# Kernel tuning notes

Hardware: AMD Instinct MI355X
Metric: run time of the kernel (lower is better)

The kernel has to match this reference:

```python
import jax, jax.numpy as jnp
import numpy as np

N_NODES = 100000
N_EDGES = 1600000
D_FEAT = 64
UNITS = [128, 128]


def setup_inputs() -> dict:
    key = jax.random.key(0)
    ks = jax.random.split(key, 8)
    row = jax.random.randint(ks[0], (N_EDGES,), 0, N_NODES, dtype=jnp.int32)
    col = jax.random.randint(ks[1], (N_EDGES,), 0, N_NODES, dtype=jnp.int32)
    vals = jax.random.uniform(ks[2], (N_EDGES,), dtype=jnp.float32)
    H = jax.random.normal(ks[3], (N_NODES, D_FEAT), dtype=jnp.float32)
    W1 = jax.random.normal(ks[4], (D_FEAT, UNITS[0]), dtype=jnp.float32) * (1.0 / np.sqrt(D_FEAT))
    b1 = jnp.zeros((UNITS[0],), dtype=jnp.float32)
    W2 = jax.random.normal(ks[5], (UNITS[0], UNITS[1]), dtype=jnp.float32) * (1.0 / np.sqrt(UNITS[0]))
    b2 = jnp.zeros((UNITS[1],), dtype=jnp.float32)
    return {"row": row, "col": col, "vals": vals, "H": H,
            "W1": W1, "b1": b1, "W2": W2, "b2": b2}


def _spmm(row, col, vals, H, n_nodes):
    # sparse A (COO) @ dense H: gather source rows, scale, scatter-add to dest
    return jax.ops.segment_sum(vals[:, None] * H[col], row, num_segments=n_nodes)


def reference(row, col, vals, H, W1, b1, W2, b2):
    n = H.shape[0]
    # layer 0: AH @ W1 + b1, relu (source bug: relu applied since i < num_units-1)
    AH = _spmm(row, col, vals, H, n)
    H1 = jax.nn.relu(AH @ W1 + b1)
    # layer 1: same structure, also relu per source's activation condition
    AH1 = _spmm(row, col, vals, H1, n)
    H2 = jax.nn.relu(AH1 @ W2 + b2)
    return H2
```

## Files before the change

kernel.cpp:

```cpp
#include <hip/hip_runtime.h>


#define NFEAT 64
#define NHID 128
#define BSHIFT 9
#define BROWS (1 << BSHIFT)
#define NB_MAX 256

typedef __attribute__((ext_vector_type(8))) short bf16x8;
typedef __attribute__((ext_vector_type(4))) float f32x4;
typedef __attribute__((ext_vector_type(2))) float f32x2;

__device__ __forceinline__ unsigned short f2bf(float x) {
  unsigned u = __float_as_uint(x);
  unsigned r = (u + 0x7FFFu + ((u >> 16) & 1u)) >> 16;
  return (unsigned short)r;
}
__device__ __forceinline__ unsigned pack2(float a, float b) {
  return (unsigned)f2bf(a) | ((unsigned)f2bf(b) << 16);
}

__device__ __forceinline__ unsigned pk_fp8x4(float a, float b, float c, float d) {
  int w = __builtin_amdgcn_cvt_pk_fp8_f32(a, b, 0, false);
  w = __builtin_amdgcn_cvt_pk_fp8_f32(c, d, w, true);
  return (unsigned)w;
}
__device__ __forceinline__ unsigned char f2fp8(float x) {
  return (unsigned char)(__builtin_amdgcn_cvt_pk_fp8_f32(x, 0.f, 0, false) & 0xFF);
}

__device__ __forceinline__ void acc16(f32x2* a, uint4 q, float v) {
  f32x2 vv = {v, v};
  a[0] += vv * __builtin_amdgcn_cvt_pk_f32_fp8(q.x, false);
  a[1] += vv * __builtin_amdgcn_cvt_pk_f32_fp8(q.x, true);
  a[2] += vv * __builtin_amdgcn_cvt_pk_f32_fp8(q.y, false);
  a[3] += vv * __builtin_amdgcn_cvt_pk_f32_fp8(q.y, true);
  a[4] += vv * __builtin_amdgcn_cvt_pk_f32_fp8(q.z, false);
  a[5] += vv * __builtin_amdgcn_cvt_pk_f32_fp8(q.z, true);
  a[6] += vv * __builtin_amdgcn_cvt_pk_f32_fp8(q.w, false);
  a[7] += vv * __builtin_amdgcn_cvt_pk_f32_fp8(q.w, true);
}

__global__ __launch_bounds__(256) void prep_kernel(
    const float* __restrict__ H, const float* __restrict__ W1,
    const float* __restrict__ W2, unsigned char* __restrict__ Hf8,
    unsigned short* __restrict__ Wsw1, unsigned short* __restrict__ Wsw2,
    int n8) {
  const int total = n8 + 64 * 128 + 128 * 128;
  for (int w = blockIdx.x * 256 + threadIdx.x; w < total; w += gridDim.x * 256) {
    if (w < n8) {
      float4 a = ((const float4*)H)[2 * w];
      float4 b = ((const float4*)H)[2 * w + 1];
      ((uint2*)Hf8)[w] = make_uint2(pk_fp8x4(a.x, a.y, a.z, a.w),
                                    pk_fp8x4(b.x, b.y, b.z, b.w));
    } else {
      int idx = w - n8;
      const float* W = W1;
      unsigned short* Wsw = Wsw1;
      if (idx >= 64 * 128) {
        idx -= 64 * 128;
        W = W2;
        Wsw = Wsw2;
      }
      int j = idx & 7, q = (idx >> 3) & 3, nn = (idx >> 5) & 127, kt = idx >> 12;
      int k = kt * 32 + q * 8 + j;
      Wsw[idx] = f2bf(W[(size_t)k * 128 + nn]);
    }
  }
}

__global__ __launch_bounds__(256) void bhist_kernel(
    const int* __restrict__ row, int* __restrict__ bcnt, int n_edges, int nb) {
  __shared__ int h[NB_MAX];
  for (int i = threadIdx.x; i < NB_MAX; i += 256) h[i] = 0;
  __syncthreads();
  for (int e = blockIdx.x * 256 + threadIdx.x; e < n_edges; e += gridDim.x * 256)
    atomicAdd(&h[row[e] >> BSHIFT], 1);
  __syncthreads();
  for (int i = threadIdx.x; i < nb; i += 256)
    if (h[i]) atomicAdd(&bcnt[i], h[i]);
}

__global__ __launch_bounds__(NB_MAX) void bscan_kernel(
    const int* __restrict__ bcnt, int* __restrict__ bbase, int* __restrict__ cur,
    int* __restrict__ row_ptr, int nb, int n) {
  __shared__ int sm[NB_MAX];
  int t = threadIdx.x;
  int v = (t < nb) ? bcnt[t] : 0;
  sm[t] = v;
  __syncthreads();
  for (int off = 1; off < NB_MAX; off <<= 1) {
    int u = (t >= off) ? sm[t - off] : 0;
    __syncthreads();
    sm[t] += u;
    __syncthreads();
  }
  if (t < nb) {
    bbase[t] = sm[t] - v;
    cur[t] = sm[t] - v;
  }
  if (t == nb - 1) {
    bbase[nb] = sm[t];
    row_ptr[n] = sm[t];
  }
}

__global__ __launch_bounds__(256) void partition_kernel(
    const int* __restrict__ row, const int* __restrict__ col,
    const float* __restrict__ vals, int* __restrict__ cur,
    int2* __restrict__ bedge, int n_edges) {
  __shared__ int h[NB_MAX], base[NB_MAX], rk[NB_MAX];
  for (int i = threadIdx.x; i < NB_MAX; i += 256) {
    h[i] = 0;
    rk[i] = 0;
  }
  __syncthreads();
  const int start = blockIdx.x * 256 + threadIdx.x;
  const int step = gridDim.x * 256;
  for (int e = start; e < n_edges; e += step)
    atomicAdd(&h[row[e] >> BSHIFT], 1);
  __syncthreads();
  for (int i = threadIdx.x; i < NB_MAX; i += 256)
    base[i] = h[i] ? atomicAdd(&cur[i], h[i]) : 0;
  __syncthreads();
  for (int e = start; e < n_edges; e += step) {
    int r = row[e];
    int b = r >> BSHIFT;
    int rl = r & (BROWS - 1);
    int p = base[b] + atomicAdd(&rk[b], 1);
    bedge[p] = make_int2((rl << 17) | col[e], __float_as_int(vals[e]));
  }
}

__global__ __launch_bounds__(512) void bucket_csr_kernel(
    const int* __restrict__ bbase, const int2* __restrict__ bedge,
    int* __restrict__ row_ptr, int2* __restrict__ sedge, int n) {
  __shared__ int cnt[BROWS];
  __shared__ int sm[BROWS];
  const int b = blockIdx.x;
  const int t = threadIdx.x;
  const int beg = bbase[b], end = bbase[b + 1];
  cnt[t] = 0;
  __syncthreads();
  for (int j = beg + t; j < end; j += 512)
    atomicAdd(&cnt[((unsigned)bedge[j].x) >> 17], 1);
  __syncthreads();
  int v = cnt[t];
  sm[t] = v;
  __syncthreads();
  for (int off = 1; off < BROWS; off <<= 1) {
    int u = (t >= off) ? sm[t - off] : 0;
    __syncthreads();
    sm[t] += u;
    __syncthreads();
  }
  {
    int incl = sm[t];
    __syncthreads();
    sm[t] = incl - v;
  }
  int r = (b << BSHIFT) + t;
  if (r < n) row_ptr[r] = beg + sm[t];
  cnt[t] = 0;
  __syncthreads();
  for (int j = beg + t; j < end; j += 512) {
    int2 ev = bedge[j];
    int rl = ((unsigned)ev.x) >> 17;
    int rank = atomicAdd(&cnt[rl], 1);
    sedge[beg + sm[rl] + rank] = make_int2(ev.x & 0x1FFFF, ev.y);
  }
}

__global__ __launch_bounds__(256) void spmm64_csr_f8(
    const int* __restrict__ row_ptr, const int2* __restrict__ sedge,
    const unsigned char* __restrict__ Hf8, unsigned short* __restrict__ outbf,
    int n) {
  int tid = blockIdx.x * 256 + threadIdx.x;
  int r = tid >> 2;
  int f = tid & 3;
  if (r >= n) return;
  const uint4* Hq = (const uint4*)Hf8;
  int beg = row_ptr[r], end = row_ptr[r + 1];
  f32x2 a[8];
#pragma unroll
  for (int i = 0; i < 8; ++i) a[i] = (f32x2){0.f, 0.f};
  int j = beg;
  if ((j & 1) && j < end) {
    int2 ev = sedge[j];
    uint4 q = Hq[ev.x * 4 + f];
    acc16(a, q, __int_as_float(ev.y));
    ++j;
  }
  for (; j + 4 <= end; j += 4) {
    int4 p0 = ((const int4*)sedge)[j >> 1];
    int4 p1 = ((const int4*)sedge)[(j >> 1) + 1];
    uint4 q0 = Hq[p0.x * 4 + f];
    uint4 q1 = Hq[p0.z * 4 + f];
    uint4 q2 = Hq[p1.x * 4 + f];
    uint4 q3 = Hq[p1.z * 4 + f];
    acc16(a, q0, __int_as_float(p0.y));
    acc16(a, q1, __int_as_float(p0.w));
    acc16(a, q2, __int_as_float(p1.y));
    acc16(a, q3, __int_as_float(p1.w));
  }
  for (; j < end; ++j) {
    int2 ev = sedge[j];
    uint4 q = Hq[ev.x * 4 + f];
    acc16(a, q, __int_as_float(ev.y));
  }
  uint4 o0 = make_uint4(pack2(a[0].x, a[0].y), pack2(a[1].x, a[1].y),
                        pack2(a[2].x, a[2].y), pack2(a[3].x, a[3].y));
  uint4 o1 = make_uint4(pack2(a[4].x, a[4].y), pack2(a[5].x, a[5].y),
                        pack2(a[6].x, a[6].y), pack2(a[7].x, a[7].y));
  ((uint4*)outbf)[(size_t)r * 8 + f * 2] = o0;
  ((uint4*)outbf)[(size_t)r * 8 + f * 2 + 1] = o1;
}

__global__ __launch_bounds__(256) void spmm128_csr_f8(
    const int* __restrict__ row_ptr, const int2* __restrict__ sedge,
    const unsigned char* __restrict__ Hf8, unsigned short* __restrict__ outbf,
    int n) {
  int tid = blockIdx.x * 256 + threadIdx.x;
  int r = tid >> 3;
  int f = tid & 7;
  if (r >= n) return;
  const uint4* Hq = (const uint4*)Hf8;
  int beg = row_ptr[r], end = row_ptr[r + 1];
  f32x2 a[8];
#pragma unroll
  for (int i = 0; i < 8; ++i) a[i] = (f32x2){0.f, 0.f};
  int j = beg;
  if ((j & 1) && j < end) {
    int2 ev = sedge[j];
    uint4 q = Hq[ev.x * 8 + f];
    acc16(a, q, __int_as_float(ev.y));
    ++j;
  }
  for (; j + 4 <= end; j += 4) {
    int4 p0 = ((const int4*)sedge)[j >> 1];
    int4 p1 = ((const int4*)sedge)[(j >> 1) + 1];
    uint4 q0 = Hq[p0.x * 8 + f];
    uint4 q1 = Hq[p0.z * 8 + f];
    uint4 q2 = Hq[p1.x * 8 + f];
    uint4 q3 = Hq[p1.z * 8 + f];
    acc16(a, q0, __int_as_float(p0.y));
    acc16(a, q1, __int_as_float(p0.w));
    acc16(a, q2, __int_as_float(p1.y));
    acc16(a, q3, __int_as_float(p1.w));
  }
  for (; j < end; ++j) {
    int2 ev = sedge[j];
    uint4 q = Hq[ev.x * 8 + f];
    acc16(a, q, __int_as_float(ev.y));
  }
  uint4 o0 = make_uint4(pack2(a[0].x, a[0].y), pack2(a[1].x, a[1].y),
                        pack2(a[2].x, a[2].y), pack2(a[3].x, a[3].y));
  uint4 o1 = make_uint4(pack2(a[4].x, a[4].y), pack2(a[5].x, a[5].y),
                        pack2(a[6].x, a[6].y), pack2(a[7].x, a[7].y));
  ((uint4*)outbf)[(size_t)r * 16 + f * 2] = o0;
  ((uint4*)outbf)[(size_t)r * 16 + f * 2 + 1] = o1;
}

template <int K, int OUTMODE>
__global__ __launch_bounds__(256) void gemm_mfma_relu(
    const unsigned short* __restrict__ Abf,
    const unsigned short* __restrict__ Wsw,
    const float* __restrict__ b, void* __restrict__ out_v, int n) {
  constexpr int KT = K / 32;
  const int lane = threadIdx.x & 63;
  const int wave = threadIdx.x >> 6;
  const int m = lane & 15;
  const int quad = lane >> 4;
  const int r0 = blockIdx.x * 64 + wave * 16;

  bf16x8 bfr[KT][8];
#pragma unroll
  for (int kt = 0; kt < KT; ++kt)
#pragma unroll
    for (int c = 0; c < 8; ++c)
      bfr[kt][c] = *(const bf16x8*)(Wsw + ((size_t)(kt * 128 + c * 16 + m)) * 32 + quad * 8);

  f32x4 acc[8];
#pragma unroll
  for (int c = 0; c < 8; ++c) acc[c] = (f32x4){0.f, 0.f, 0.f, 0.f};

  int row = r0 + m;
  if (row >= n) row = n - 1;
  const uint4* Arow = (const uint4*)(Abf + (size_t)row * K);
#pragma unroll
  for (int kt = 0; kt < KT; ++kt) {
    bf16x8 a = *(const bf16x8*)&Arow[kt * 4 + quad];
#pragma unroll
    for (int c = 0; c < 8; ++c)
      acc[c] = __builtin_amdgcn_mfma_f32_16x16x32_bf16(a, bfr[kt][c], acc[c], 0, 0, 0);
  }

#pragma unroll
  for (int c = 0; c < 8; ++c) {
    float bias = b[c * 16 + m];
#pragma unroll
    for (int i = 0; i < 4; ++i) {
      int rr = r0 + quad * 4 + i;
      if (rr >= n) continue;
      float v = fmaxf(acc[c][i] + bias, 0.f);
      if (OUTMODE == 2)
        ((unsigned char*)out_v)[(size_t)rr * 128 + c * 16 + m] = f2fp8(v);
      else
        ((float*)out_v)[(size_t)rr * 128 + c * 16 + m] = v;
    }
  }
}

__global__ __launch_bounds__(256) void spmm64_atomic(
    const int* __restrict__ row, const int* __restrict__ col,
    const float* __restrict__ vals, const float* __restrict__ Hin,
    float* __restrict__ out, int n_edges) {
  int tid = blockIdx.x * 256 + threadIdx.x;
  int e = tid >> 4, f = tid & 15;
  if (e >= n_edges) return;
  int c = col[e], r = row[e];
  float v = vals[e];
  float4 h = ((const float4*)Hin)[(size_t)c * 16 + f];
  float* o = out + (size_t)r * 64 + f * 4;
  atomicAdd(o + 0, v * h.x);
  atomicAdd(o + 1, v * h.y);
  atomicAdd(o + 2, v * h.z);
  atomicAdd(o + 3, v * h.w);
}

__global__ __launch_bounds__(256) void spmm128_atomic(
    const int* __restrict__ row, const int* __restrict__ col,
    const float* __restrict__ vals, const float* __restrict__ Hin,
    float* __restrict__ out, int n_edges) {
  int tid = blockIdx.x * 256 + threadIdx.x;
  int e = tid >> 5, f = tid & 31;
  if (e >= n_edges) return;
  int c = col[e], r = row[e];
  float v = vals[e];
  float4 h = ((const float4*)Hin)[(size_t)c * 32 + f];
  float* o = out + (size_t)r * 128 + f * 4;
  atomicAdd(o + 0, v * h.x);
  atomicAdd(o + 1, v * h.y);
  atomicAdd(o + 2, v * h.z);
  atomicAdd(o + 3, v * h.w);
}

template <int K>
__global__ __launch_bounds__(256) void gemm_tiled_relu(
    const float* __restrict__ A, const float* __restrict__ W,
    const float* __restrict__ b, float* __restrict__ out, int n) {
  constexpr int KB = 32;
  constexpr int RP = 132;
  __shared__ float As[KB][RP];
  __shared__ float Ws[KB][128];
  const int t = threadIdx.x;
  const int tx = t & 15, ty = t >> 4;
  const int r0 = blockIdx.x * 128;
  float4 acc0[8], acc1[8];
#pragma unroll
  for (int i = 0; i < 8; ++i) {
    acc0[i] = make_float4(0.f, 0.f, 0.f, 0.f);
    acc1[i] = make_float4(0.f, 0.f, 0.f, 0.f);
  }
  for (int k0 = 0; k0 < K; k0 += KB) {
#pragma unroll
    for (int q = 0; q < 4; ++q) {
      int f = q * 256 + t;
      int kk = f >> 5, cv = f & 31;
      ((float4*)&Ws[kk][0])[cv] = ((const float4*)(W + (size_t)(k0 + kk) * 128))[cv];
    }
#pragma unroll
    for (int q = 0; q < 4; ++q) {
      int f = q * 256 + t;
      int r = f >> 3, kv = f & 7;
      float4 av = make_float4(0.f, 0.f, 0.f, 0.f);
      if (r0 + r < n) av = ((const float4*)(A + (size_t)(r0 + r) * K + k0))[kv];
      As[4 * kv + 0][r] = av.x;
      As[4 * kv + 1][r] = av.y;
      As[4 * kv + 2][r] = av.z;
      As[4 * kv + 3][r] = av.w;
    }
    __syncthreads();
#pragma unroll
    for (int k = 0; k < KB; ++k) {
      float4 w0 = *((const float4*)&Ws[k][4 * tx]);
      float4 w1 = *((const float4*)&Ws[k][64 + 4 * tx]);
#pragma unroll
      for (int i = 0; i < 8; ++i) {
        float a = As[k][ty + 16 * i];
        acc0[i].x = fmaf(a, w0.x, acc0[i].x);
        acc0[i].y = fmaf(a, w0.y, acc0[i].y);
        acc0[i].z = fmaf(a, w0.z, acc0[i].z);
        acc0[i].w = fmaf(a, w0.w, acc0[i].w);
        acc1[i].x = fmaf(a, w1.x, acc1[i].x);
        acc1[i].y = fmaf(a, w1.y, acc1[i].y);
        acc1[i].z = fmaf(a, w1.z, acc1[i].z);
        acc1[i].w = fmaf(a, w1.w, acc1[i].w);
      }
    }
    __syncthreads();
  }
  float4 bb0 = ((const float4*)b)[tx];
  float4 bb1 = ((const float4*)(b + 64))[tx];
#pragma unroll
  for (int i = 0; i < 8; ++i) {
    int r = r0 + ty + 16 * i;
    if (r >= n) continue;
    float4 o0, o1;
    o0.x = fmaxf(acc0[i].x + bb0.x, 0.f);
    o0.y = fmaxf(acc0[i].y + bb0.y, 0.f);
    o0.z = fmaxf(acc0[i].z + bb0.z, 0.f);
    o0.w = fmaxf(acc0[i].w + bb0.w, 0.f);
    o1.x = fmaxf(acc1[i].x + bb1.x, 0.f);
    o1.y = fmaxf(acc1[i].y + bb1.y, 0.f);
    o1.z = fmaxf(acc1[i].z + bb1.z, 0.f);
    o1.w = fmaxf(acc1[i].w + bb1.w, 0.f);
    ((float4*)(out + (size_t)r * 128))[tx] = o0;
    ((float4*)(out + (size_t)r * 128 + 64))[tx] = o1;
  }
}

extern "C" void kernel_launch(void* const* d_in, const int* in_sizes, int n_in,
                              void* d_out, int out_size, void* d_ws, size_t ws_size,
                              hipStream_t stream) {
  const int* row = (const int*)d_in[0];
  const int* col = (const int*)d_in[1];
  const float* vals = (const float*)d_in[2];
  const float* H = (const float*)d_in[3];
  const float* W1 = (const float*)d_in[4];
  const float* b1 = (const float*)d_in[5];
  const float* W2 = (const float*)d_in[6];
  const float* b2 = (const float*)d_in[7];
  float* out = (float*)d_out;

  const int n_edges = in_sizes[0];
  const int n_nodes = in_sizes[3] / NFEAT;
  const int nb = (n_nodes + BROWS - 1) / BROWS;
  const int mfma_grid = (n_nodes + 63) / 64;

  size_t off = 0;
  char* base = (char*)d_ws;
  char* slab0 = base;
  size_t slab0_sz = (size_t)n_edges * 8;
  size_t ah1_sz = (size_t)n_nodes * NHID * 2;
  if (ah1_sz > slab0_sz) slab0_sz = ah1_sz;
  off += slab0_sz;
  unsigned char* Hf8 = (unsigned char*)(base + off);   off += (size_t)n_nodes * NFEAT;
  unsigned char* H1f8 = (unsigned char*)(base + off);  off += (size_t)n_nodes * NHID;
  unsigned short* AHbf = (unsigned short*)(base + off); off += (size_t)n_nodes * NFEAT * 2;
  int2* sedge = (int2*)(base + off);  off += (size_t)n_edges * 8;
  unsigned short* Wsw1 = (unsigned short*)(base + off); off += 64 * 128 * 2;
  unsigned short* Wsw2 = (unsigned short*)(base + off); off += 128 * 128 * 2;
  int* bcnt = (int*)(base + off);     off += NB_MAX * 4;
  int* bbase = (int*)(base + off);    off += (NB_MAX + 1) * 4;
  int* cur = (int*)(base + off);      off += NB_MAX * 4;
  int* row_ptr = (int*)(base + off);  off += ((size_t)n_nodes + 1) * 4;
  const size_t needed = off;
  int2* bedge = (int2*)slab0;
  unsigned short* AH1bf = (unsigned short*)slab0;

  if (ws_size >= needed && nb <= NB_MAX && n_nodes <= (1 << 17)) {
    hipMemsetAsync(bcnt, 0, NB_MAX * sizeof(int), stream);
    bhist_kernel<<<256, 256, 0, stream>>>(row, bcnt, n_edges, nb);
    bscan_kernel<<<1, NB_MAX, 0, stream>>>(bcnt, bbase, cur, row_ptr, nb, n_nodes);
    partition_kernel<<<256, 256, 0, stream>>>(row, col, vals, cur, bedge, n_edges);
    bucket_csr_kernel<<<nb, 512, 0, stream>>>(bbase, bedge, row_ptr, sedge, n_nodes);

    prep_kernel<<<1024, 256, 0, stream>>>(H, W1, W2, Hf8, Wsw1, Wsw2,
                                          n_nodes * NFEAT / 8);

    spmm64_csr_f8<<<(n_nodes * 4 + 255) / 256, 256, 0, stream>>>(
        row_ptr, sedge, Hf8, AHbf, n_nodes);
    gemm_mfma_relu<64, 2><<<mfma_grid, 256, 0, stream>>>(
        AHbf, Wsw1, b1, H1f8, n_nodes);
    spmm128_csr_f8<<<(n_nodes * 8 + 255) / 256, 256, 0, stream>>>(
        row_ptr, sedge, H1f8, AH1bf, n_nodes);
    gemm_mfma_relu<128, 0><<<mfma_grid, 256, 0, stream>>>(
        AH1bf, Wsw2, b2, out, n_nodes);
  } else {
    float* fAH = (float*)d_ws;
    float* fH1 = fAH + (size_t)n_nodes * NFEAT;
    hipMemsetAsync(fAH, 0, (size_t)n_nodes * NFEAT * sizeof(float), stream);
    hipMemsetAsync(out, 0, (size_t)n_nodes * NHID * sizeof(float), stream);
    spmm64_atomic<<<(n_edges * 16 + 255) / 256, 256, 0, stream>>>(row, col, vals, H, fAH, n_edges);
    gemm_tiled_relu<64><<<(n_nodes + 127) / 128, 256, 0, stream>>>(fAH, W1, b1, fH1, n_nodes);
    spmm128_atomic<<<(n_edges * 32 + 255) / 256, 256, 0, stream>>>(row, col, vals, fH1, out, n_edges);
    gemm_tiled_relu<128><<<(n_nodes + 127) / 128, 256, 0, stream>>>(out, W2, b2, out, n_nodes);
  }
}
```

Before: 280.3 us.

## Build CSR via global per-row atomic histogram, three-pass scan, and atomic scatter

```diff
diff --git a/kernel.cpp b/kernel.cpp
--- a/kernel.cpp
+++ b/kernel.cpp
@@ -3,9 +3,8 @@
 
 #define NFEAT 64
 #define NHID 128
-#define BSHIFT 9
-#define BROWS (1 << BSHIFT)
-#define NB_MAX 256
+#define CHUNK 1024
+#define NC_MAX 1024
 
 typedef __attribute__((ext_vector_type(8))) short bf16x8;
 typedef __attribute__((ext_vector_type(4))) float f32x4;
@@ -69,105 +68,112 @@
   }
 }
 
-__global__ __launch_bounds__(256) void bhist_kernel(
-    const int* __restrict__ row, int* __restrict__ bcnt, int n_edges, int nb) {
-  __shared__ int h[NB_MAX];
-  for (int i = threadIdx.x; i < NB_MAX; i += 256) h[i] = 0;
+__global__ __launch_bounds__(256) void rhist_kernel(
+    const int* __restrict__ row, int* __restrict__ cnt, int n_edges) {
+  int e = (blockIdx.x * 256 + threadIdx.x) * 4;
+  if (e + 4 <= n_edges) {
+    int4 r4 = *(const int4*)(row + e);
+    atomicAdd(&cnt[r4.x], 1);
+    atomicAdd(&cnt[r4.y], 1);
+    atomicAdd(&cnt[r4.z], 1);
+    atomicAdd(&cnt[r4.w], 1);
+  } else {
+    for (; e < n_edges; ++e) atomicAdd(&cnt[row[e]], 1);
+  }
+}
+
+__global__ __launch_bounds__(256) void scan1_kernel(
+    const int* __restrict__ cnt, int* __restrict__ rp, int* __restrict__ bsum) {
+  __shared__ int sm[256];
+  const int b = blockIdx.x, t = threadIdx.x;
+  int4 c = ((const int4*)cnt)[b * 256 + t];
+  int s = c.x + c.y + c.z + c.w;
+  sm[t] = s;
   __syncthreads();
-  for (int e = blockIdx.x * 256 + threadIdx.x; e < n_edges; e += gridDim.x * 256)
-    atomicAdd(&h[row[e] >> BSHIFT], 1);
+  for (int off = 1; off < 256; off <<= 1) {
+    int u = (t >= off) ? sm[t - off] : 0;
+    __syncthreads();
+    sm[t] += u;
+    __syncthreads();
+  }
+  int excl = sm[t] - s;
+  int4 o;
+  o.x = excl;
+  o.y = o.x + c.x;
+  o.z = o.y + c.y;
+  o.w = o.z + c.z;
+  ((int4*)rp)[b * 256 + t] = o;
+  if (t == 255) bsum[b] = sm[255];
+}
+
+__global__ __launch_bounds__(256) void scan2_kernel(int* __restrict__ bsum, int nc) {
+  __shared__ int sm[256];
+  const int t = threadIdx.x;
+  const int base = t * 4;
+  int v0 = (base + 0 < nc) ? bsum[base + 0] : 0;
+  int v1 = (base + 1 < nc) ? bsum[base + 1] : 0;
+  int v2 = (base + 2 < nc) ? bsum[base + 2] : 0;
+  int v3 = (base + 3 < nc) ? bsum[base + 3] : 0;
+  int s = v0 + v1 + v2 + v3;
+  sm[t] = s;
   __syncthreads();
-  for (int i = threadIdx.x; i < nb; i += 256)
-    if (h[i]) atomicAdd(&bcnt[i], h[i]);
-}
-
-__global__ __launch_bounds__(NB_MAX) void bscan_kernel(
-    const int* __restrict__ bcnt, int* __restrict__ bbase, int* __restrict__ cur,
-    int* __restrict__ row_ptr, int nb, int n) {
-  __shared__ int sm[NB_MAX];
-  int t = threadIdx.x;
-  int v = (t < nb) ? bcnt[t] : 0;
-  sm[t] = v;
-  __syncthreads();
-  for (int off = 1; off < NB_MAX; off <<= 1) {
+  for (int off = 1; off < 256; off <<= 1) {
     int u = (t >= off) ? sm[t - off] : 0;
     __syncthreads();
     sm[t] += u;
     __syncthreads();
   }
-  if (t < nb) {
-    bbase[t] = sm[t] - v;
-    cur[t] = sm[t] - v;
-  }
-  if (t == nb - 1) {
-    bbase[nb] = sm[t];
-    row_ptr[n] = sm[t];
-  }
-}
-
-__global__ __launch_bounds__(256) void partition_kernel(
+  int excl = sm[t] - s;
+  if (base + 0 < nc) bsum[base + 0] = excl;
+  if (base + 1 < nc) bsum[base + 1] = excl + v0;
+  if (base + 2 < nc) bsum[base + 2] = excl + v0 + v1;
+  if (base + 3 < nc) bsum[base + 3] = excl + v0 + v1 + v2;
+  if (t == 255) bsum[nc] = sm[255];
+}
+
+__global__ __launch_bounds__(256) void scan3_kernel(
+    int* __restrict__ rp, int* __restrict__ cur, const int* __restrict__ bsum,
+    int n, int nc) {
+  int t = blockIdx.x * 256 + threadIdx.x;
+  if (t == 0) rp[n] = bsum[nc];
+  int i = t * 4;
+  if (i + 4 <= n) {
+    int add = bsum[i >> 10];
+    int4 v = *(const int4*)(rp + i);
+    v.x += add; v.y += add; v.z += add; v.w += add;
+    *(int4*)(rp + i) = v;
+    *(int4*)(cur + i) = v;
+  } else {
+    for (; i < n; ++i) {
+      int v = rp[i] + bsum[i >> 10];
+      rp[i] = v;
+      cur[i] = v;
+    }
+  }
+}
+
+__global__ __launch_bounds__(256) void scatter_kernel(
     const int* __restrict__ row, const int* __restrict__ col,
     const float* __restrict__ vals, int* __restrict__ cur,
-    int2* __restrict__ bedge, int n_edges) {
-  __shared__ int h[NB_MAX], base[NB_MAX], rk[NB_MAX];
-  for (int i = threadIdx.x; i < NB_MAX; i += 256) {
-    h[i] = 0;
-    rk[i] = 0;
-  }
-  __syncthreads();
-  const int start = blockIdx.x * 256 + threadIdx.x;
-  const int step = gridDim.x * 256;
-  for (int e = start; e < n_edges; e += step)
-    atomicAdd(&h[row[e] >> BSHIFT], 1);
-  __syncthreads();
-  for (int i = threadIdx.x; i < NB_MAX; i += 256)
-    base[i] = h[i] ? atomicAdd(&cur[i], h[i]) : 0;
-  __syncthreads();
-  for (int e = start; e < n_edges; e += step) {
-    int r = row[e];
-    int b = r >> BSHIFT;
-    int rl = r & (BROWS - 1);
-    int p = base[b] + atomicAdd(&rk[b], 1);
-    bedge[p] = make_int2((rl << 17) | col[e], __float_as_int(vals[e]));
-  }
-}
-
-__global__ __launch_bounds__(512) void bucket_csr_kernel(
-    const int* __restrict__ bbase, const int2* __restrict__ bedge,
-    int* __restrict__ row_ptr, int2* __restrict__ sedge, int n) {
-  __shared__ int cnt[BROWS];
-  __shared__ int sm[BROWS];
-  const int b = blockIdx.x;
-  const int t = threadIdx.x;
-  const int beg = bbase[b], end = bbase[b + 1];
-  cnt[t] = 0;
-  __syncthreads();
-  for (int j = beg + t; j < end; j += 512)
-    atomicAdd(&cnt[((unsigned)bedge[j].x) >> 17], 1);
-  __syncthreads();
-  int v = cnt[t];
-  sm[t] = v;
-  __syncthreads();
-  for (int off = 1; off < BROWS; off <<= 1) {
-    int u = (t >= off) ? sm[t - off] : 0;
-    __syncthreads();
-    sm[t] += u;
-    __syncthreads();
-  }
-  {
-    int incl = sm[t];
-    __syncthreads();
-    sm[t] = incl - v;
-  }
-  int r = (b << BSHIFT) + t;
-  if (r < n) row_ptr[r] = beg + sm[t];
-  cnt[t] = 0;
-  __syncthreads();
-  for (int j = beg + t; j < end; j += 512) {
-    int2 ev = bedge[j];
-    int rl = ((unsigned)ev.x) >> 17;
-    int rank = atomicAdd(&cnt[rl], 1);
-    sedge[beg + sm[rl] + rank] = make_int2(ev.x & 0x1FFFF, ev.y);
+    int2* __restrict__ sedge, int n_edges) {
+  int e = (blockIdx.x * 256 + threadIdx.x) * 4;
+  if (e + 4 <= n_edges) {
+    int4 r4 = *(const int4*)(row + e);
+    int4 c4 = *(const int4*)(col + e);
+    float4 v4 = *(const float4*)(vals + e);
+    int p0 = atomicAdd(&cur[r4.x], 1);
+    int p1 = atomicAdd(&cur[r4.y], 1);
+    int p2 = atomicAdd(&cur[r4.z], 1);
+    int p3 = atomicAdd(&cur[r4.w], 1);
+    sedge[p0] = make_int2(c4.x, __float_as_int(v4.x));
+    sedge[p1] = make_int2(c4.y, __float_as_int(v4.y));
+    sedge[p2] = make_int2(c4.z, __float_as_int(v4.z));
+    sedge[p3] = make_int2(c4.w, __float_as_int(v4.w));
+  } else {
+    for (; e < n_edges; ++e) {
+      int p = atomicAdd(&cur[row[e]], 1);
+      sedge[p] = make_int2(col[e], __float_as_int(vals[e]));
+    }
   }
 }
 
@@ -435,36 +441,33 @@
 
   const int n_edges = in_sizes[0];
   const int n_nodes = in_sizes[3] / NFEAT;
-  const int nb = (n_nodes + BROWS - 1) / BROWS;
+  const int nc = (n_nodes + CHUNK - 1) >> 10;
+  const int npad = nc << 10;
   const int mfma_grid = (n_nodes + 63) / 64;
 
   size_t off = 0;
   char* base = (char*)d_ws;
-  char* slab0 = base;
-  size_t slab0_sz = (size_t)n_edges * 8;
-  size_t ah1_sz = (size_t)n_nodes * NHID * 2;
-  if (ah1_sz > slab0_sz) slab0_sz = ah1_sz;
-  off += slab0_sz;
+  unsigned short* AH1bf = (unsigned short*)(base + off); off += (size_t)n_nodes * NHID * 2;
   unsigned char* Hf8 = (unsigned char*)(base + off);   off += (size_t)n_nodes * NFEAT;
   unsigned char* H1f8 = (unsigned char*)(base + off);  off += (size_t)n_nodes * NHID;
   unsigned short* AHbf = (unsigned short*)(base + off); off += (size_t)n_nodes * NFEAT * 2;
   int2* sedge = (int2*)(base + off);  off += (size_t)n_edges * 8;
   unsigned short* Wsw1 = (unsigned short*)(base + off); off += 64 * 128 * 2;
   unsigned short* Wsw2 = (unsigned short*)(base + off); off += 128 * 128 * 2;
-  int* bcnt = (int*)(base + off);     off += NB_MAX * 4;
-  int* bbase = (int*)(base + off);    off += (NB_MAX + 1) * 4;
-  int* cur = (int*)(base + off);      off += NB_MAX * 4;
-  int* row_ptr = (int*)(base + off);  off += ((size_t)n_nodes + 1) * 4;
+  int* row_ptr = (int*)(base + off);  off += ((size_t)npad + 4) * 4;
+  int* cur = (int*)(base + off);      off += (size_t)npad * 4;
+  int* bsum = (int*)(base + off);     off += (NC_MAX + 1) * 4;
   const size_t needed = off;
-  int2* bedge = (int2*)slab0;
-  unsigned short* AH1bf = (unsigned short*)slab0;
-
-  if (ws_size >= needed && nb <= NB_MAX && n_nodes <= (1 << 17)) {
-    hipMemsetAsync(bcnt, 0, NB_MAX * sizeof(int), stream);
-    bhist_kernel<<<256, 256, 0, stream>>>(row, bcnt, n_edges, nb);
-    bscan_kernel<<<1, NB_MAX, 0, stream>>>(bcnt, bbase, cur, row_ptr, nb, n_nodes);
-    partition_kernel<<<256, 256, 0, stream>>>(row, col, vals, cur, bedge, n_edges);
-    bucket_csr_kernel<<<nb, 512, 0, stream>>>(bbase, bedge, row_ptr, sedge, n_nodes);
+
+  if (ws_size >= needed && nc <= NC_MAX) {
+    hipMemsetAsync(cur, 0, (size_t)npad * 4, stream);
+    const int egrid = (n_edges + 1023) / 1024;
+    rhist_kernel<<<egrid, 256, 0, stream>>>(row, cur, n_edges);
+    scan1_kernel<<<nc, 256, 0, stream>>>(cur, row_ptr, bsum);
+    scan2_kernel<<<1, 256, 0, stream>>>(bsum, nc);
+    scan3_kernel<<<(n_nodes + 1023) / 1024, 256, 0, stream>>>(
+        row_ptr, cur, bsum, n_nodes, nc);
+    scatter_kernel<<<egrid, 256, 0, stream>>>(row, col, vals, cur, sedge, n_edges);
 
     prep_kernel<<<1024, 256, 0, stream>>>(H, W1, W2, Hf8, Wsw1, Wsw2,
                                           n_nodes * NFEAT / 8);
```

Result: slower. 405.8 us (+44.8%).
